# Performance work log

Measured on AMD Instinct MI355X. Metric: run time of the kernel, lower is better.

The kernel has to match this reference:

```python
import jax, jax.numpy as jnp
import numpy as np

N_NODES = 100000
N_EDGES = 3200000
NUM_CLASSES = 10
SQRT3 = 3.0 ** 0.5


def setup_inputs() -> dict:
    key = jax.random.key(0)
    ks = jax.random.split(key, 20)
    f32 = jnp.float32
    return {
        "positions": jax.random.normal(ks[0], (N_NODES, 3), f32) * 5.0,
        "edge_src": jax.random.randint(ks[1], (N_EDGES,), 0, N_NODES, jnp.int32),
        "edge_dst": jax.random.randint(ks[2], (N_EDGES,), 0, N_NODES, jnp.int32),
        # layer1: TP('1x0e', sh) -> '1x0e + 1x1o' -> Linear -> '5x0e + 5x1o'
        "W0_1": jax.random.normal(ks[3], (5, 1), f32),
        "W1_1": jax.random.normal(ks[4], (5, 1, 3), f32),
        "b_1": jax.random.normal(ks[5], (5,), f32),
        # gate1: Linear('5x0e+5x1o' -> '10x0e') uses only the 5 input 0e irreps
        "Wg1": jax.random.normal(ks[6], (10, 5), f32),
        "bg1": jax.random.normal(ks[7], (10,), f32),
        # layer2: TP('5x0e+5x1o', sh) -> 10x0e + 10x1o (+5x1e unused) -> '5x0e+5x1o'
        "W0_2": jax.random.normal(ks[8], (5, 10), f32),
        "W1_2": jax.random.normal(ks[9], (5, 10, 3), f32),
        "b_2": jax.random.normal(ks[10], (5,), f32),
        "Wg2": jax.random.normal(ks[11], (10, 5), f32),
        "bg2": jax.random.normal(ks[12], (10,), f32),
        # layer3: TP -> 10x0e used -> '5x0e'
        "W0_3": jax.random.normal(ks[13], (5, 10), f32),
        "b_3": jax.random.normal(ks[14], (5,), f32),
        "Wg3": jax.random.normal(ks[15], (10, 5), f32),
        "bg3": jax.random.normal(ks[16], (10,), f32),
        "Wout": jax.random.normal(ks[17], (NUM_CLASSES, 5), f32) * 0.3,
        "bout": jax.random.normal(ks[18], (NUM_CLASSES,), f32) * 0.1,
    }


def _sh1(rel):
    # component-normalized real spherical harmonics, lmax=1: Y0 = 1, Y1 = sqrt(3)*r_hat
    r = jnp.linalg.norm(rel, axis=-1, keepdims=True)
    return SQRT3 * rel / jnp.maximum(r, 1e-9)  # [E,3]


def _scatter_mean(x, dst, n):
    s = jax.ops.segment_sum(x, dst, num_segments=n)
    cnt = jax.ops.segment_sum(jnp.ones((x.shape[0],), x.dtype), dst, num_segments=n)
    cnt = jnp.maximum(cnt, 1.0).reshape((n,) + (1,) * (x.ndim - 1))
    return s / cnt


def _layer(s, v, sh1, dst, n, W0, b, W1=None):
    # per-edge CG tensor product of dest-node features with edge SH, then linear, then scatter-mean
    sd = s[dst]                                            # [E,a0] gather 0e feats
    tp_s = [sd]                                            # 0e x 0e(Y0=1) -> 0e
    if v is not None:
        vd = v[dst]                                        # [E,a1,3] gather 1o feats
        tp_s.append(jnp.einsum('eic,ec->ei', vd, sh1) / SQRT3)  # 1o x 1o -> 0e (CG dot)
    tp_s = jnp.concatenate(tp_s, axis=1)
    out_s = _scatter_mean(tp_s @ W0.T + b, dst, n)         # [N,out0]
    if W1 is None:
        return out_s, None
    tp_v = [sd[:, :, None] * sh1[:, None, :]]              # 0e x 1o -> 1o
    if v is not None:
        tp_v.append(vd)                                    # 1o x 0e(Y0=1) -> 1o
    tp_v = jnp.concatenate(tp_v, axis=1)                   # [E,in1,3]
    out_v = _scatter_mean(jnp.einsum('eic,oic->eoc', tp_v, W1), dst, n)
    return out_s, out_v


def _gate(s, v, Wg, bg):
    # ActivationLayer: gate each irrep by GELU of a learned scalar (torch GELU = exact erf)
    g = jax.nn.gelu(s @ Wg.T + bg, approximate=False)
    n0 = s.shape[1]
    gs = g[:, :n0] * s
    if v is None:
        return gs, None
    return gs, g[:, n0:n0 + v.shape[1], None] * v


def reference(positions, edge_src, edge_dst, W0_1, W1_1, b_1, Wg1, bg1,
              W0_2, W1_2, b_2, Wg2, bg2, W0_3, b_3, Wg3, bg3, Wout, bout):
    n = positions.shape[0]
    rel = positions[edge_dst] - positions[edge_src]
    sh1 = _sh1(rel)
    s = jnp.ones((n, 1), positions.dtype)  # dummy '1x0e' starting node features
    s, v = _layer(s, None, sh1, edge_dst, n, W0_1, b_1, W1_1)
    s, v = _gate(s, v, Wg1, bg1)
    s, v = _layer(s, v, sh1, edge_dst, n, W0_2, b_2, W1_2)
    s, v = _gate(s, v, Wg2, bg2)
    s, _ = _layer(s, v, sh1, edge_dst, n, W0_3, b_3, None)
    s, _ = _gate(s, None, Wg3, bg3)
    pooled = jnp.mean(s, axis=0)                       # avg over nodes -> [5]
    return jax.nn.softmax(pooled @ Wout.T + bout)      # [NUM_CLASSES]
```

## Files before the change

### kernel.cpp

```cpp
#include <hip/hip_runtime.h>
#include <math.h>

#define SQRT3F 1.7320508075688772f
#define INV_SQRT3F 0.57735026918962576f
typedef unsigned long long u64;
typedef unsigned int u32;

#define PK_SCALE 1024.0f
#define PK_MASK  0x7FFFFull

#define NPR2   2048
#define NRG2   49
#define REP2   ((size_t)NRG2 * NPR2)
#define EPB    4096

#define NPR    4096
#define NRANGE 25

__device__ __forceinline__ float gelu_exact(float x) {
    return 0.5f * x * (1.0f + erff(x * 0.70710678118654752f));
}

__device__ __forceinline__ u64 sh_to_w(float rx, float ry, float rz) {
    float rr = sqrtf(rx*rx + ry*ry + rz*rz);
    float inv = (SQRT3F * PK_SCALE) / fmaxf(rr, 1e-9f);
    u32 ax = (u32)__float2int_rn(rx * inv) + 2048u;
    u32 ay = (u32)__float2int_rn(ry * inv) + 2048u;
    u32 az = (u32)__float2int_rn(rz * inv) + 2048u;
    return (u64)ax | ((u64)ay << 19) | ((u64)az << 38) | (1ull << 57);
}

__global__ __launch_bounds__(256) void pack_pos_kernel(
    const float* __restrict__ pos, float4* __restrict__ pos4,
    u32* __restrict__ done, int N)
{
    int i = blockIdx.x * 256 + threadIdx.x;
    if (i < N) pos4[i] = make_float4(pos[3*i], pos[3*i+1], pos[3*i+2], 0.f);
    if (blockIdx.x == 0 && threadIdx.x == 0) *done = 0;
}

__global__ __launch_bounds__(1024) void scatter_kernel(
    const int* __restrict__ src, const int* __restrict__ dst,
    u32* __restrict__ gbuf, u32* __restrict__ cnts, int E)
{
    __shared__ u32 hist[NRG2];
    __shared__ u32 base[NRG2];
    __shared__ u32 place[NRG2];
    __shared__ u32 recbuf[EPB];
    const int p = blockIdx.x;
    if (threadIdx.x < NRG2) hist[threadIdx.x] = 0;
    __syncthreads();

    const int start = p * EPB;
    int end = start + EPB;
    if (end > E) end = E;

    int nk = 0;
    int d[4], s[4], r[4];
    u32 rec[4];
    int i0 = start + (int)threadIdx.x * 4;
    if (i0 + 4 <= end) {
        int4 d4 = *reinterpret_cast<const int4*>(dst + i0);
        int4 s4 = *reinterpret_cast<const int4*>(src + i0);
        d[0]=d4.x; d[1]=d4.y; d[2]=d4.z; d[3]=d4.w;
        s[0]=s4.x; s[1]=s4.y; s[2]=s4.z; s[3]=s4.w;
        nk = 4;
    } else if (i0 < end) {
        nk = end - i0;
        for (int k = 0; k < nk; ++k) { d[k] = dst[i0+k]; s[k] = src[i0+k]; }
    }
    for (int k = 0; k < nk; ++k) {
        r[k] = d[k] >> 11;
        rec[k] = ((u32)s[k] << 11) | ((u32)d[k] & 2047u);
    }
    for (int k = 0; k < nk; ++k) atomicAdd(&hist[r[k]], 1u);
    __syncthreads();

    if (threadIdx.x == 0) {
        u32 acc = 0;
        for (int j = 0; j < NRG2; ++j) { base[j] = acc; acc += hist[j]; }
    }
    __syncthreads();
    if (threadIdx.x < NRG2) place[threadIdx.x] = base[threadIdx.x];
    __syncthreads();

    for (int k = 0; k < nk; ++k) {
        u32 idx = atomicAdd(&place[r[k]], 1u);
        recbuf[idx] = rec[k];
    }
    __syncthreads();

    const int total = end - start;
    u32* out = gbuf + (size_t)p * EPB;
    for (int j = threadIdx.x; j < total; j += 1024) out[j] = recbuf[j];
    if (threadIdx.x < NRG2)
        cnts[p * NRG2 + threadIdx.x] = (base[threadIdx.x] << 16) | hist[threadIdx.x];
}

__global__ __launch_bounds__(512) void gather_kernel(
    const float4* __restrict__ pos4,
    const u32* __restrict__ gbuf, const u32* __restrict__ cnts,
    u64* __restrict__ reps, int P, int R2, int N)
{
    __shared__ u64 bins[NPR2];
    __shared__ float4 posl[NPR2];
    __shared__ u32 segn[256];
    const int r  = blockIdx.x % NRG2;
    const int c2 = blockIdx.x / NRG2;
    const int base = r * NPR2;

    for (int j = threadIdx.x; j < NPR2; j += 512) {
        bins[j] = 0;
        int g = base + j;
        posl[j] = (g < N) ? pos4[g] : make_float4(0.f, 0.f, 0.f, 0.f);
    }
    const int nseg = (P - c2 + R2 - 1) / R2;
    for (int t = threadIdx.x; t < nseg; t += 512)
        segn[t] = cnts[(c2 + t * R2) * NRG2 + r];
    __syncthreads();

    const int wid = threadIdx.x >> 6, lane = threadIdx.x & 63;
    for (int sgi = wid; sgi < nseg; sgi += 8) {
        const int p = c2 + sgi * R2;
        const u32 bc = segn[sgi];
        const u32 n = bc & 0xFFFFu;
        const u32* seg = gbuf + (size_t)p * EPB + (bc >> 16);
        for (u32 t = lane; t < n; t += 64) {
            u32 rec = seg[t];
            u32 j = rec & 2047u, ss = rec >> 11;
            float4 ps = pos4[ss];
            float4 pd = posl[j];
            atomicAdd(&bins[j], sh_to_w(pd.x - ps.x, pd.y - ps.y, pd.z - ps.z));
        }
    }
    __syncthreads();

    u64* outp = reps + (size_t)c2 * REP2 + base;
    for (int j = threadIdx.x; j < NPR2; j += 512) outp[j] = bins[j];
}

__global__ __launch_bounds__(256, 4) void edge_bin_kernel(
    const float* __restrict__ pos,
    const int* __restrict__ src,
    const int* __restrict__ dst,
    u64* __restrict__ reps, int E, int span)
{
    __shared__ u64 bins[NPR];
    __shared__ u32 q[4][128];
    const int g = blockIdx.x;
    const int xcd = g & 7;
    const int slot = g >> 3;
    const int c = xcd + 8 * (slot / NRANGE);
    const int r = slot % NRANGE;
    const int base = r * NPR;
    const int lane = threadIdx.x & 63;
    const int wid  = threadIdx.x >> 6;
    const u64 ltmask = (1ull << lane) - 1ull;

    for (int j = threadIdx.x; j < NPR; j += 256) bins[j] = 0;
    __syncthreads();

    const int start = c * span;
    int end = start + span;
    if (end > E) end = E;
    const int niter = (end > start) ? ((end - start + 1023) >> 10) : 0;
    int qcount = 0;

    auto process = [&](u32 i2) {
        int s2 = src[i2]; int d2 = dst[i2];
        u32 j = (u32)(d2 - base);
        atomicAdd(&bins[j], sh_to_w(pos[3*d2+0]-pos[3*s2+0],
                                    pos[3*d2+1]-pos[3*s2+1],
                                    pos[3*d2+2]-pos[3*s2+2]));
    };

    for (int t = 0; t < niter; ++t) {
        int i0 = start + ((int)threadIdx.x << 2) + (t << 10);
        int4 d4 = make_int4(-1, -1, -1, -1);
        if (i0 + 4 <= end) d4 = *reinterpret_cast<const int4*>(dst + i0);
        else if (i0 < end) for (int k = 0; i0 + k < end; ++k) (&d4.x)[k] = dst[i0 + k];
        #pragma unroll
        for (int k = 0; k < 4; ++k) {
            int i = i0 + k;
            bool in = (i < end) && ((u32)((&d4.x)[k] - base) < NPR);
            u64 mask = __ballot(in);
            if (in) q[wid][qcount + __popcll(mask & ltmask)] = (u32)i;
            qcount += (int)__popcll(mask);
            if (qcount >= 64) { qcount -= 64; process(q[wid][qcount + lane]); }
        }
    }
    if (lane < qcount) process(q[wid][lane]);
    __syncthreads();

    u64* outp = reps + (size_t)c * ((size_t)NRANGE * NPR) + base;
    for (int j = threadIdx.x; j < NPR; j += 256) outp[j] = bins[j];
}

template<bool FUSE>
__global__ __launch_bounds__(256) void node_kernel(
    const u64* __restrict__ reps, size_t repStride, int R,
    const float* __restrict__ W0_1, const float* __restrict__ W1_1, const float* __restrict__ b_1,
    const float* __restrict__ Wg1,  const float* __restrict__ bg1,
    const float* __restrict__ W0_2, const float* __restrict__ W1_2, const float* __restrict__ b_2,
    const float* __restrict__ Wg2,  const float* __restrict__ bg2,
    const float* __restrict__ W0_3, const float* __restrict__ b_3,
    const float* __restrict__ Wg3,  const float* __restrict__ bg3,
    float* __restrict__ partials, int N,
    const float* __restrict__ Wout, const float* __restrict__ bout,
    float* __restrict__ out, float invN, u32* __restrict__ done)
{
    int d = blockIdx.x * blockDim.x + threadIdx.x;
    float sf[5] = {0.f, 0.f, 0.f, 0.f, 0.f};

    if (d < N) {
        u64 w = 0;
        int r = 0;
        for (; r + 4 <= R; r += 4) {
            u64 a0 = reps[(size_t)(r+0) * repStride + (u32)d];
            u64 a1 = reps[(size_t)(r+1) * repStride + (u32)d];
            u64 a2 = reps[(size_t)(r+2) * repStride + (u32)d];
            u64 a3 = reps[(size_t)(r+3) * repStride + (u32)d];
            w += a0 + a1 + a2 + a3;
        }
        for (; r < R; ++r) w += reps[(size_t)r * repStride + (u32)d];
        u32 deg = (u32)(w >> 57);
        if (deg > 0) {
            long long bias = (long long)deg << 11;
            float invdS = 1.0f / (PK_SCALE * (float)deg);
            float m[3];
            m[0] = (float)((long long)( w        & PK_MASK) - bias) * invdS;
            m[1] = (float)((long long)((w >> 19) & PK_MASK) - bias) * invdS;
            m[2] = (float)((long long)((w >> 38) & PK_MASK) - bias) * invdS;

            float s1[5], v1[5][3];
            #pragma unroll
            for (int i = 0; i < 5; ++i) {
                s1[i] = W0_1[i] + b_1[i];
                #pragma unroll
                for (int c = 0; c < 3; ++c) v1[i][c] = W1_1[i*3+c] * m[c];
            }
            float g1[10];
            #pragma unroll
            for (int j = 0; j < 10; ++j) {
                float t = bg1[j];
                #pragma unroll
                for (int i = 0; i < 5; ++i) t += Wg1[j*5+i] * s1[i];
                g1[j] = gelu_exact(t);
            }
            #pragma unroll
            for (int i = 0; i < 5; ++i) {
                s1[i] *= g1[i];
                #pragma unroll
                for (int c = 0; c < 3; ++c) v1[i][c] *= g1[5+i];
            }

            float dot1[5];
            #pragma unroll
            for (int i = 0; i < 5; ++i)
                dot1[i] = (v1[i][0]*m[0] + v1[i][1]*m[1] + v1[i][2]*m[2]) * INV_SQRT3F;
            float s2[5];
            #pragma unroll
            for (int o = 0; o < 5; ++o) {
                float t = b_2[o];
                #pragma unroll
                for (int i = 0; i < 5; ++i) t += W0_2[o*10+i] * s1[i];
                #pragma unroll
                for (int i = 0; i < 5; ++i) t += W0_2[o*10+5+i] * dot1[i];
                s2[o] = t;
            }
            float v2[5][3];
            #pragma unroll
            for (int o = 0; o < 5; ++o) {
                #pragma unroll
                for (int c = 0; c < 3; ++c) {
                    float t = 0.f;
                    #pragma unroll
                    for (int i = 0; i < 5; ++i) {
                        t += W1_2[(o*10+i)*3+c]   * (s1[i] * m[c]);
                        t += W1_2[(o*10+5+i)*3+c] * v1[i][c];
                    }
                    v2[o][c] = t;
                }
            }
            float g2[10];
            #pragma unroll
            for (int j = 0; j < 10; ++j) {
                float t = bg2[j];
                #pragma unroll
                for (int i = 0; i < 5; ++i) t += Wg2[j*5+i] * s2[i];
                g2[j] = gelu_exact(t);
            }
            #pragma unroll
            for (int i = 0; i < 5; ++i) {
                s2[i] *= g2[i];
                #pragma unroll
                for (int c = 0; c < 3; ++c) v2[i][c] *= g2[5+i];
            }

            float dot2[5];
            #pragma unroll
            for (int i = 0; i < 5; ++i)
                dot2[i] = (v2[i][0]*m[0] + v2[i][1]*m[1] + v2[i][2]*m[2]) * INV_SQRT3F;
            float s3[5];
            #pragma unroll
            for (int o = 0; o < 5; ++o) {
                float t = b_3[o];
                #pragma unroll
                for (int i = 0; i < 5; ++i) t += W0_3[o*10+i] * s2[i];
                #pragma unroll
                for (int i = 0; i < 5; ++i) t += W0_3[o*10+5+i] * dot2[i];
                s3[o] = t;
            }
            #pragma unroll
            for (int i = 0; i < 5; ++i) {
                float t = bg3[i];
                #pragma unroll
                for (int j = 0; j < 5; ++j) t += Wg3[i*5+j] * s3[j];
                sf[i] = gelu_exact(t) * s3[i];
            }
        }
    }

    #pragma unroll
    for (int k = 0; k < 5; ++k) {
        float v = sf[k];
        for (int off = 32; off > 0; off >>= 1) v += __shfl_down(v, off);
        sf[k] = v;
    }
    __shared__ float lred[4][5];
    __shared__ int islast;
    int wid = threadIdx.x >> 6, lane = threadIdx.x & 63;
    if (lane == 0) {
        #pragma unroll
        for (int k = 0; k < 5; ++k) lred[wid][k] = sf[k];
    }
    __syncthreads();
    if (threadIdx.x == 0) {
        #pragma unroll
        for (int k = 0; k < 5; ++k)
            partials[blockIdx.x * 5 + k] = lred[0][k] + lred[1][k] + lred[2][k] + lred[3][k];
    }

    if (FUSE) {
        if (threadIdx.x == 0) {
            __threadfence();
            u32 old = atomicAdd(done, 1u);
            islast = (old == gridDim.x - 1);
        }
        __syncthreads();
        if (!islast) return;
        __threadfence();
        float s[5] = {0.f, 0.f, 0.f, 0.f, 0.f};
        for (int b = threadIdx.x; b < (int)gridDim.x; b += 256) {
            #pragma unroll
            for (int k = 0; k < 5; ++k) s[k] += partials[b * 5 + k];
        }
        #pragma unroll
        for (int k = 0; k < 5; ++k) {
            float v = s[k];
            for (int off = 32; off > 0; off >>= 1) v += __shfl_down(v, off);
            s[k] = v;
        }
        __syncthreads();
        if (lane == 0) {
            #pragma unroll
            for (int k = 0; k < 5; ++k) lred[wid][k] = s[k];
        }
        __syncthreads();
        if (threadIdx.x == 0) {
            float pooled[5];
            #pragma unroll
            for (int i = 0; i < 5; ++i)
                pooled[i] = (lred[0][i] + lred[1][i] + lred[2][i] + lred[3][i]) * invN;
            float lg[10], mx = -1e30f;
            #pragma unroll
            for (int j = 0; j < 10; ++j) {
                float t = bout[j];
                #pragma unroll
                for (int i = 0; i < 5; ++i) t += Wout[j*5+i] * pooled[i];
                lg[j] = t;
                mx = fmaxf(mx, t);
            }
            float se = 0.f;
            #pragma unroll
            for (int j = 0; j < 10; ++j) { lg[j] = expf(lg[j] - mx); se += lg[j]; }
            float inv = 1.0f / se;
            #pragma unroll
            for (int j = 0; j < 10; ++j) out[j] = lg[j] * inv;
        }
    }
}

__global__ __launch_bounds__(256) void finalize_kernel(
    const float* __restrict__ partials, int nb,
    const float* __restrict__ Wout, const float* __restrict__ bout,
    float* __restrict__ out, float invN)
{
    float s[5] = {0.f, 0.f, 0.f, 0.f, 0.f};
    for (int b = threadIdx.x; b < nb; b += 256) {
        #pragma unroll
        for (int k = 0; k < 5; ++k) s[k] += partials[b * 5 + k];
    }
    #pragma unroll
    for (int k = 0; k < 5; ++k) {
        float v = s[k];
        for (int off = 32; off > 0; off >>= 1) v += __shfl_down(v, off);
        s[k] = v;
    }
    __shared__ float lred[4][5];
    int wid = threadIdx.x >> 6, lane = threadIdx.x & 63;
    if (lane == 0) {
        #pragma unroll
        for (int k = 0; k < 5; ++k) lred[wid][k] = s[k];
    }
    __syncthreads();
    if (threadIdx.x == 0) {
        float pooled[5];
        #pragma unroll
        for (int i = 0; i < 5; ++i)
            pooled[i] = (lred[0][i] + lred[1][i] + lred[2][i] + lred[3][i]) * invN;
        float lg[10], mx = -1e30f;
        #pragma unroll
        for (int j = 0; j < 10; ++j) {
            float t = bout[j];
            #pragma unroll
            for (int i = 0; i < 5; ++i) t += Wout[j*5+i] * pooled[i];
            lg[j] = t;
            mx = fmaxf(mx, t);
        }
        float se = 0.f;
        #pragma unroll
        for (int j = 0; j < 10; ++j) { lg[j] = expf(lg[j] - mx); se += lg[j]; }
        float inv = 1.0f / se;
        #pragma unroll
        for (int j = 0; j < 10; ++j) out[j] = lg[j] * inv;
    }
}

extern "C" void kernel_launch(void* const* d_in, const int* in_sizes, int n_in,
                              void* d_out, int out_size, void* d_ws, size_t ws_size,
                              hipStream_t stream) {
    const float* pos  = (const float*)d_in[0];
    const int*   esrc = (const int*)d_in[1];
    const int*   edst = (const int*)d_in[2];
    const float* W0_1 = (const float*)d_in[3];
    const float* W1_1 = (const float*)d_in[4];
    const float* b_1  = (const float*)d_in[5];
    const float* Wg1  = (const float*)d_in[6];
    const float* bg1  = (const float*)d_in[7];
    const float* W0_2 = (const float*)d_in[8];
    const float* W1_2 = (const float*)d_in[9];
    const float* b_2  = (const float*)d_in[10];
    const float* Wg2  = (const float*)d_in[11];
    const float* bg2  = (const float*)d_in[12];
    const float* W0_3 = (const float*)d_in[13];
    const float* b_3  = (const float*)d_in[14];
    const float* Wg3  = (const float*)d_in[15];
    const float* bg3  = (const float*)d_in[16];
    const float* Wout = (const float*)d_in[17];
    const float* bout = (const float*)d_in[18];

    const int N = in_sizes[0] / 3;
    const int E = in_sizes[1];
    const int nblocks = (N + 255) / 256;
    const int P = (E + EPB - 1) / EPB;

    {
        const int r2c[3] = {16, 8, 4};
        for (int a = 0; a < 3; ++a) {
            int R2 = r2c[a];
            size_t off = 16384;
            size_t o_ctr  = off; off += 256;
            size_t o_pos4 = off; off += ((size_t)N * 16 + 255) & ~(size_t)255;
            size_t o_reps = off; off += (size_t)R2 * REP2 * 8;
            size_t o_cnts = off; off += ((size_t)P * NRG2 * 4 + 255) & ~(size_t)255;
            size_t o_gbuf = off; off += (size_t)P * EPB * 4;
            if (off > ws_size) continue;

            float*  partials = (float*)d_ws;
            u32*    done     = (u32*)((char*)d_ws + o_ctr);
            float4* pos4     = (float4*)((char*)d_ws + o_pos4);
            u64*    reps     = (u64*)((char*)d_ws + o_reps);
            u32*    cnts     = (u32*)((char*)d_ws + o_cnts);
            u32*    gbuf     = (u32*)((char*)d_ws + o_gbuf);

            pack_pos_kernel<<<nblocks, 256, 0, stream>>>(pos, pos4, done, N);
            scatter_kernel<<<P, 1024, 0, stream>>>(esrc, edst, gbuf, cnts, E);
            gather_kernel<<<NRG2 * R2, 512, 0, stream>>>(pos4, gbuf, cnts,
                reps, P, R2, N);
            node_kernel<true><<<nblocks, 256, 0, stream>>>(reps, REP2, R2,
                W0_1, W1_1, b_1, Wg1, bg1,
                W0_2, W1_2, b_2, Wg2, bg2,
                W0_3, b_3, Wg3, bg3,
                partials, N, Wout, bout, (float*)d_out, 1.0f / (float)N, done);
            return;
        }
    }

    {
        float* partials = (float*)d_ws;
        u64* reps = (u64*)((char*)d_ws + 16384);
        const size_t repStride = (size_t)NRANGE * NPR;
        size_t avail = ws_size > 16384 ? ws_size - 16384 : 0;
        int C = (int)(avail / (repStride * 8));
        if (C > 48) C = 48;
        C &= ~7;
        if (C >= 8) {
            int span = (int)((((size_t)E + C - 1) / C + 3) & ~(size_t)3);
            edge_bin_kernel<<<NRANGE * C, 256, 0, stream>>>(pos, esrc, edst, reps, E, span);
            node_kernel<false><<<nblocks, 256, 0, stream>>>(reps, repStride, C,
                W0_1, W1_1, b_1, Wg1, bg1,
                W0_2, W1_2, b_2, Wg2, bg2,
                W0_3, b_3, Wg3, bg3,
                partials, N, nullptr, nullptr, nullptr, 0.f, nullptr);
            finalize_kernel<<<1, 256, 0, stream>>>(partials, nblocks, Wout, bout,
                                                   (float*)d_out, 1.0f / (float)N);
        }
    }
}
```

Baseline: 74.35 us.

## Fuse position packing into scatter kernel and streamline gather loop

Merges the position-packing kernel into the edge scatter kernel as extra blocks, removing one kernel launch. Replaces the serial single-thread prefix sum over the range histogram with a wavefront shuffle scan. In the gather kernel, drops the LDS copy of destination positions and reads them straight from global memory, which frees LDS so more blocks can fit. The inner loop is also unrolled by two to keep more gathers in flight. The trade-off is extra global/L2 traffic for destination positions and more register pressure.

```diff
diff --git a/kernel.cpp b/kernel.cpp
--- a/kernel.cpp
+++ b/kernel.cpp
@@ -30,24 +30,24 @@
     return (u64)ax | ((u64)ay << 19) | ((u64)az << 38) | (1ull << 57);
 }
 
-__global__ __launch_bounds__(256) void pack_pos_kernel(
+__global__ __launch_bounds__(1024) void scatter_pack_kernel(
     const float* __restrict__ pos, float4* __restrict__ pos4,
-    u32* __restrict__ done, int N)
+    const int* __restrict__ src, const int* __restrict__ dst,
+    u32* __restrict__ gbuf, u32* __restrict__ cnts, u32* __restrict__ done,
+    int E, int N, int P)
 {
-    int i = blockIdx.x * 256 + threadIdx.x;
-    if (i < N) pos4[i] = make_float4(pos[3*i], pos[3*i+1], pos[3*i+2], 0.f);
-    if (blockIdx.x == 0 && threadIdx.x == 0) *done = 0;
-}
-
-__global__ __launch_bounds__(1024) void scatter_kernel(
-    const int* __restrict__ src, const int* __restrict__ dst,
-    u32* __restrict__ gbuf, u32* __restrict__ cnts, int E)
-{
+    const int p = blockIdx.x;
+    if (p >= P) {
+        int i = (p - P) * 1024 + (int)threadIdx.x;
+        if (i < N) pos4[i] = make_float4(pos[3*i], pos[3*i+1], pos[3*i+2], 0.f);
+        if (p == P && threadIdx.x == 0) *done = 0;
+        return;
+    }
+
     __shared__ u32 hist[NRG2];
     __shared__ u32 base[NRG2];
     __shared__ u32 place[NRG2];
     __shared__ u32 recbuf[EPB];
-    const int p = blockIdx.x;
     if (threadIdx.x < NRG2) hist[threadIdx.x] = 0;
     __syncthreads();
 
@@ -76,12 +76,17 @@
     for (int k = 0; k < nk; ++k) atomicAdd(&hist[r[k]], 1u);
     __syncthreads();
 
-    if (threadIdx.x == 0) {
-        u32 acc = 0;
-        for (int j = 0; j < NRG2; ++j) { base[j] = acc; acc += hist[j]; }
-    }
-    __syncthreads();
-    if (threadIdx.x < NRG2) place[threadIdx.x] = base[threadIdx.x];
+    if (threadIdx.x < 64) {
+        int lane = threadIdx.x;
+        u32 h = (lane < NRG2) ? hist[lane] : 0;
+        u32 v = h;
+        #pragma unroll
+        for (int off = 1; off < 64; off <<= 1) {
+            u32 t = __shfl_up(v, off);
+            if (lane >= off) v += t;
+        }
+        if (lane < NRG2) { base[lane] = v - h; place[lane] = v - h; }
+    }
     __syncthreads();
 
     for (int k = 0; k < nk; ++k) {
@@ -97,23 +102,19 @@
         cnts[p * NRG2 + threadIdx.x] = (base[threadIdx.x] << 16) | hist[threadIdx.x];
 }
 
-__global__ __launch_bounds__(512) void gather_kernel(
+__global__ __launch_bounds__(512, 8) void gather_kernel(
     const float4* __restrict__ pos4,
     const u32* __restrict__ gbuf, const u32* __restrict__ cnts,
     u64* __restrict__ reps, int P, int R2, int N)
 {
     __shared__ u64 bins[NPR2];
-    __shared__ float4 posl[NPR2];
     __shared__ u32 segn[256];
     const int r  = blockIdx.x % NRG2;
     const int c2 = blockIdx.x / NRG2;
     const int base = r * NPR2;
-
-    for (int j = threadIdx.x; j < NPR2; j += 512) {
-        bins[j] = 0;
-        int g = base + j;
-        posl[j] = (g < N) ? pos4[g] : make_float4(0.f, 0.f, 0.f, 0.f);
-    }
+    const float4* posd = pos4 + base;
+
+    for (int j = threadIdx.x; j < NPR2; j += 512) bins[j] = 0;
     const int nseg = (P - c2 + R2 - 1) / R2;
     for (int t = threadIdx.x; t < nseg; t += 512)
         segn[t] = cnts[(c2 + t * R2) * NRG2 + r];
@@ -125,12 +126,19 @@
         const u32 bc = segn[sgi];
         const u32 n = bc & 0xFFFFu;
         const u32* seg = gbuf + (size_t)p * EPB + (bc >> 16);
-        for (u32 t = lane; t < n; t += 64) {
-            u32 rec = seg[t];
-            u32 j = rec & 2047u, ss = rec >> 11;
-            float4 ps = pos4[ss];
-            float4 pd = posl[j];
-            atomicAdd(&bins[j], sh_to_w(pd.x - ps.x, pd.y - ps.y, pd.z - ps.z));
+        for (u32 t = lane; t < n; t += 128) {
+            u32 rec0 = seg[t];
+            bool h1 = (t + 64) < n;
+            u32 rec1 = h1 ? seg[t + 64] : 0;
+            u32 j0 = rec0 & 2047u, s0 = rec0 >> 11;
+            float4 ps0 = pos4[s0];
+            float4 pd0 = posd[j0];
+            u32 j1 = rec1 & 2047u, s1 = rec1 >> 11;
+            float4 ps1, pd1;
+            if (h1) { ps1 = pos4[s1]; pd1 = posd[j1]; }
+            atomicAdd(&bins[j0], sh_to_w(pd0.x-ps0.x, pd0.y-ps0.y, pd0.z-ps0.z));
+            if (h1)
+                atomicAdd(&bins[j1], sh_to_w(pd1.x-ps1.x, pd1.y-ps1.y, pd1.z-ps1.z));
         }
     }
     __syncthreads();
@@ -464,6 +472,7 @@
     const int E = in_sizes[1];
     const int nblocks = (N + 255) / 256;
     const int P = (E + EPB - 1) / EPB;
+    const int packBlocks = (N + 1023) / 1024;
 
     {
         const int r2c[3] = {16, 8, 4};
@@ -484,8 +493,8 @@
             u32*    cnts     = (u32*)((char*)d_ws + o_cnts);
             u32*    gbuf     = (u32*)((char*)d_ws + o_gbuf);
 
-            pack_pos_kernel<<<nblocks, 256, 0, stream>>>(pos, pos4, done, N);
-            scatter_kernel<<<P, 1024, 0, stream>>>(esrc, edst, gbuf, cnts, E);
+            scatter_pack_kernel<<<P + packBlocks, 1024, 0, stream>>>(
+                pos, pos4, esrc, edst, gbuf, cnts, done, E, N, P);
             gather_kernel<<<NRG2 * R2, 512, 0, stream>>>(pos4, gbuf, cnts,
                 reps, P, R2, N);
             node_kernel<true><<<nblocks, 256, 0, stream>>>(reps, REP2, R2,
```

Measured after the change: 74.22 us, median of 2. Within noise of the previous version (-0.2%).
